# Kernel tuning notes

Hardware: AMD Instinct MI355X
Metric: run time of the kernel (lower is better)

Reference implementation:

```python
import jax, jax.numpy as jnp
import numpy as np

B, CH, IMG, P = 16, 3, 384, 16
D, HEADS, DH, MLP, DEPTH = 384, 6, 64, 1536, 6
INNER = HEADS * DH
PD = P * P * 5 * CH          # SPT patch dim = 3840
GRID = IMG // P              # 24
NP = GRID * GRID             # 576 patches
SEQ = NP + 1                 # +cls = 577


def layer_norm(x, g, b, eps=1e-5):
    mu = jnp.mean(x, axis=-1, keepdims=True)
    var = jnp.var(x, axis=-1, keepdims=True)
    return (x - mu) * jax.lax.rsqrt(var + eps) * g + b


def spt_shifts(x):
    # F.pad semantics: (left,right,top,bottom) with negative = crop
    s1 = jnp.pad(x, ((0, 0), (0, 0), (0, 0), (1, 0)))[:, :, :, :-1]  # (1,-1,0,0)
    s2 = jnp.pad(x, ((0, 0), (0, 0), (0, 0), (0, 1)))[:, :, :, 1:]   # (-1,1,0,0)
    s3 = jnp.pad(x, ((0, 0), (0, 0), (1, 0), (0, 0)))[:, :, :-1, :]  # (0,0,1,-1)
    s4 = jnp.pad(x, ((0, 0), (0, 0), (0, 1), (0, 0)))[:, :, 1:, :]   # (0,0,-1,1)
    return jnp.concatenate([x, s1, s2, s3, s4], axis=1)  # [b, 5c, H, W]


def patchify(x):
    # 'b c (h p1) (w p2) -> b (h w) (p1 p2 c)'
    b, c, _, _ = x.shape
    x = x.reshape(b, c, GRID, P, GRID, P)
    x = x.transpose(0, 2, 4, 3, 5, 1)  # b h w p1 p2 c
    return x.reshape(b, GRID * GRID, P * P * c)


def setup_inputs():
    key = jax.random.key(0)
    ks = jax.random.split(key, 16)
    img = jax.random.normal(ks[0], (B, CH, IMG, IMG), jnp.float32)
    spt_g = jnp.ones((PD,), jnp.float32)
    spt_b = jnp.zeros((PD,), jnp.float32)
    spt_w = jax.random.normal(ks[1], (PD, D), jnp.float32) * (1.0 / np.sqrt(PD))
    spt_bias = jnp.zeros((D,), jnp.float32)
    pos = jax.random.normal(ks[2], (1, SEQ, D), jnp.float32) * 0.02
    cls = jax.random.normal(ks[3], (1, 1, D), jnp.float32) * 0.02
    attn_g = jnp.ones((DEPTH, D), jnp.float32)
    attn_b = jnp.zeros((DEPTH, D), jnp.float32)
    temp = jnp.full((DEPTH,), np.log(DH ** -0.5), jnp.float32)
    wqkv = jax.random.normal(ks[4], (DEPTH, D, 3 * INNER), jnp.float32) * 0.02
    wout = jax.random.normal(ks[5], (DEPTH, INNER, D), jnp.float32) * 0.02
    bout = jnp.zeros((DEPTH, D), jnp.float32)
    ff_g = jnp.ones((DEPTH, D), jnp.float32)
    ff_b = jnp.zeros((DEPTH, D), jnp.float32)
    w1 = jax.random.normal(ks[6], (DEPTH, D, MLP), jnp.float32) * 0.02
    b1 = jnp.zeros((DEPTH, MLP), jnp.float32)
    w2 = jax.random.normal(ks[7], (DEPTH, MLP, D), jnp.float32) * 0.02
    b2 = jnp.zeros((DEPTH, D), jnp.float32)
    return {"img": img, "spt_g": spt_g, "spt_b": spt_b, "spt_w": spt_w,
            "spt_bias": spt_bias, "pos": pos, "cls": cls, "attn_g": attn_g,
            "attn_b": attn_b, "temp": temp, "wqkv": wqkv, "wout": wout,
            "bout": bout, "ff_g": ff_g, "ff_b": ff_b, "w1": w1, "b1": b1,
            "w2": w2, "b2": b2}


def vit_forward(img, spt_g, spt_b, spt_w, spt_bias, pos, cls, attn_g, attn_b,
                temp, wqkv, wout, bout, ff_g, ff_b, w1, b1, w2, b2):
    # SPT patch embedding
    x = patchify(spt_shifts(img))                      # [b, NP, PD]
    x = layer_norm(x, spt_g, spt_b) @ spt_w + spt_bias  # [b, NP, D]
    b = x.shape[0]
    cls_tok = jnp.broadcast_to(cls, (b, 1, D))
    x = jnp.concatenate([cls_tok, x], axis=1) + pos[:, :SEQ]

    eye = jnp.eye(SEQ, dtype=bool)
    neg = -jnp.finfo(x.dtype).max

    def block(x, p):
        ag, ab, t, wq, wo, bo, fg, fb, W1, B1, W2, B2 = p
        h = layer_norm(x, ag, ab)
        qkv = h @ wq                                   # [b, n, 3*inner]
        q, k, v = jnp.split(qkv, 3, axis=-1)
        q = q.reshape(b, SEQ, HEADS, DH).transpose(0, 2, 1, 3)
        k = k.reshape(b, SEQ, HEADS, DH).transpose(0, 2, 1, 3)
        v = v.reshape(b, SEQ, HEADS, DH).transpose(0, 2, 1, 3)
        dots = jnp.einsum('bhid,bhjd->bhij', q, k) * jnp.exp(t)
        dots = jnp.where(eye, neg, dots)               # diagonal mask (LSA)
        attn = jax.nn.softmax(dots, axis=-1)
        out = jnp.einsum('bhij,bhjd->bhid', attn, v)
        out = out.transpose(0, 2, 1, 3).reshape(b, SEQ, INNER)
        x = out @ wo + bo + x
        h = layer_norm(x, fg, fb)
        x = jax.nn.gelu(h @ W1 + B1, approximate=False) @ W2 + B2 + x
        return x, None

    params = (attn_g, attn_b, temp, wqkv, wout, bout, ff_g, ff_b, w1, b1, w2, b2)
    x, _ = jax.lax.scan(block, x, params)
    return x


def reference(img, spt_g, spt_b, spt_w, spt_bias, pos, cls, attn_g, attn_b,
              temp, wqkv, wout, bout, ff_g, ff_b, w1, b1, w2, b2):
    return vit_forward(img, spt_g, spt_b, spt_w, spt_bias, pos, cls, attn_g,
                       attn_b, temp, wqkv, wout, bout, ff_g, ff_b, w1, b1,
                       w2, b2)
```

## Files before the change

kernel.cpp:

```cpp
#include <hip/hip_runtime.h>

typedef unsigned short ushort_t;
typedef __bf16 bf16x8 __attribute__((ext_vector_type(8)));
typedef float f32x4 __attribute__((ext_vector_type(4)));

#define SEQ_ 577
#define D_ 384
#define NTOK (16 * 577)

enum { M_QKV = 0, M_OUT, M_MLP1, M_MLP2 };

__device__ inline float b2f(ushort_t u) {
    unsigned int x = ((unsigned int)u) << 16;
    float f; __builtin_memcpy(&f, &x, 4); return f;
}
__device__ inline ushort_t f2b(float f) {
    unsigned int x; __builtin_memcpy(&x, &f, 4);
    x = x + 0x7fffu + ((x >> 16) & 1u);
    return (ushort_t)(x >> 16);
}

__device__ void transpose_tile(const float* __restrict__ src,
                               ushort_t* __restrict__ dst,
                               int ldn, int ldk, int k0, int n0)
{
    __shared__ float t[64][65];
    const int tid = threadIdx.x;
    const int c = tid & 63, rr = tid >> 6;
#pragma unroll
    for (int i = 0; i < 16; i++) {
        int kl = rr + i * 4;
        t[kl][c] = src[(size_t)(k0 + kl) * ldn + n0 + c];
    }
    __syncthreads();
#pragma unroll
    for (int i = 0; i < 16; i++) {
        int nl = rr + i * 4;
        dst[(size_t)(n0 + nl) * ldk + k0 + c] = f2b(t[c][nl]);
    }
}

__global__ __launch_bounds__(256) void prep_spt_kernel(
    const float* __restrict__ w, ushort_t* __restrict__ wt)
{
    transpose_tile(w, wt, 384, 3840, blockIdx.x * 64, blockIdx.y * 64);
}

__global__ __launch_bounds__(256) void prep_all_kernel(
    const float* __restrict__ wqkv, const float* __restrict__ wout,
    const float* __restrict__ w1, const float* __restrict__ w2,
    ushort_t* __restrict__ W6)
{
    int id = blockIdx.x;
    int l = id / 432;
    int r = id - l * 432;
    ushort_t* qkv_t  = W6 + (size_t)l * 1769472;
    ushort_t* wout_t = qkv_t + 442368;
    ushort_t* w1_t   = wout_t + 147456;
    ushort_t* w2_t   = w1_t + 589824;
    const float* wq = wqkv + (size_t)l * 442368;
    const float* wo = wout + (size_t)l * 147456;
    const float* W1 = w1 + (size_t)l * 589824;
    const float* W2 = w2 + (size_t)l * 589824;
    if (r < 108) {
        int kt = r / 18, nt = r % 18;
        transpose_tile(wq, qkv_t, 1152, 384, kt * 64, nt * 64);
    } else if (r < 144) {
        r -= 108; int kt = r / 6, nt = r % 6;
        transpose_tile(wo, wout_t, 384, 384, kt * 64, nt * 64);
    } else if (r < 288) {
        r -= 144; int kt = r / 24, nt = r % 24;
        transpose_tile(W1, w1_t, 1536, 384, kt * 64, nt * 64);
    } else {
        r -= 288; int kt = r / 6, nt = r % 6;
        transpose_tile(W2, w2_t, 384, 1536, kt * 64, nt * 64);
    }
}

template <int MODE>
__global__ __launch_bounds__(256) void gemm128(
    const ushort_t* __restrict__ A, const ushort_t* __restrict__ Bt,
    ushort_t* __restrict__ Co, float* __restrict__ resid,
    const float* __restrict__ bias,
    int M, int K, int ldc)
{
    __shared__ __align__(16) ushort_t As[128][40];
    __shared__ __align__(16) ushort_t Bs[128][40];

    const int tid = threadIdx.x;
    const int rowBase = blockIdx.y * 128;
    const int colBase = blockIdx.x * 128;
    const int nk = K >> 5;

    const int lr = tid >> 2, lk = (tid & 3) * 8;
    const int wv = tid >> 6, lane = tid & 63;
    const int wm = (wv >> 1) * 64, wn = (wv & 1) * 64;
    const int m16 = lane & 15, q4 = lane >> 4, kb = q4 * 8;

    const ushort_t* pa0 = A + (size_t)(rowBase + lr) * K + lk;
    const ushort_t* pa1 = pa0 + (size_t)64 * K;
    const ushort_t* pb0 = Bt + (size_t)(colBase + lr) * K + lk;
    const ushort_t* pb1 = pb0 + (size_t)64 * K;

    f32x4 acc[4][4];
#pragma unroll
    for (int i = 0; i < 4; i++)
#pragma unroll
        for (int j = 0; j < 4; j++) acc[i][j] = (f32x4){0.f, 0.f, 0.f, 0.f};

    uint4 xa0 = *(const uint4*)pa0,        xa1 = *(const uint4*)pa1;
    uint4 xb0 = *(const uint4*)pb0,        xb1 = *(const uint4*)pb1;
    uint4 ya0 = *(const uint4*)(pa0 + 32), ya1 = *(const uint4*)(pa1 + 32);
    uint4 yb0 = *(const uint4*)(pb0 + 32), yb1 = *(const uint4*)(pb1 + 32);

    auto stage = [&](uint4& ra0, uint4& ra1, uint4& rb0, uint4& rb1, int ktNext) {
        __syncthreads();
        *(uint4*)&As[lr][lk] = ra0;
        *(uint4*)&As[64 + lr][lk] = ra1;
        *(uint4*)&Bs[lr][lk] = rb0;
        *(uint4*)&Bs[64 + lr][lk] = rb1;
        __syncthreads();
        if (ktNext < nk) {
            int off = ktNext * 32;
            ra0 = *(const uint4*)(pa0 + off);
            ra1 = *(const uint4*)(pa1 + off);
            rb0 = *(const uint4*)(pb0 + off);
            rb1 = *(const uint4*)(pb1 + off);
        }
        bf16x8 af[4], bf[4];
#pragma unroll
        for (int mt = 0; mt < 4; mt++) af[mt] = *(const bf16x8*)&As[wm + mt * 16 + m16][kb];
#pragma unroll
        for (int nt = 0; nt < 4; nt++) bf[nt] = *(const bf16x8*)&Bs[wn + nt * 16 + m16][kb];
#pragma unroll
        for (int mt = 0; mt < 4; mt++)
#pragma unroll
            for (int nt = 0; nt < 4; nt++)
                acc[mt][nt] = __builtin_amdgcn_mfma_f32_16x16x32_bf16(af[mt], bf[nt], acc[mt][nt], 0, 0, 0);
    };

    for (int kt = 0; kt < nk; kt += 2) {
        stage(xa0, xa1, xb0, xb1, kt + 2);
        stage(ya0, ya1, yb0, yb1, kt + 3);
    }

#pragma unroll
    for (int mt = 0; mt < 4; mt++)
#pragma unroll
        for (int nt = 0; nt < 4; nt++) {
            int col = colBase + wn + nt * 16 + m16;
#pragma unroll
            for (int r = 0; r < 4; r++) {
                int row = rowBase + wm + mt * 16 + q4 * 4 + r;
                if (row >= M) continue;
                float v = acc[mt][nt][r];
                if (MODE == M_QKV) {
                    Co[(size_t)row * ldc + col] = f2b(v);
                } else if (MODE == M_MLP1) {
                    float t = v + bias[col];
                    float gl = 0.5f * t * (1.0f + erff(t * 0.70710678118f));
                    Co[(size_t)row * ldc + col] = f2b(gl);
                } else if (MODE == M_OUT || MODE == M_MLP2) {
                    size_t o = (size_t)row * ldc + col;
                    resid[o] = resid[o] + v + bias[col];
                }
            }
        }
}

__global__ __launch_bounds__(256) void gemm64_spt(
    const ushort_t* __restrict__ A, const ushort_t* __restrict__ Bt,
    float* __restrict__ resid, const float* __restrict__ bias,
    const float* __restrict__ pos, int M, int K, int rowOff)
{
    __shared__ __align__(16) ushort_t As[64][40];
    __shared__ __align__(16) ushort_t Bs[64][40];

    const int tid = threadIdx.x;
    const int rowBase = blockIdx.y * 64;
    const int colBase = blockIdx.x * 64;
    const int nk = K >> 5;
    const int lr = tid >> 2, lk = (tid & 3) * 8;
    const int wv = tid >> 6, lane = tid & 63;
    const int wm = (wv >> 1) * 32, wn = (wv & 1) * 32;
    const int m16 = lane & 15, q4 = lane >> 4, kb = q4 * 8;

    const ushort_t* pa = A + (size_t)(rowBase + lr) * K + lk;
    const ushort_t* pb = Bt + (size_t)(colBase + lr) * K + lk;

    f32x4 acc[2][2];
#pragma unroll
    for (int i = 0; i < 2; i++)
#pragma unroll
        for (int j = 0; j < 2; j++) acc[i][j] = (f32x4){0.f, 0.f, 0.f, 0.f};

    uint4 xa = *(const uint4*)pa,        xb = *(const uint4*)pb;
    uint4 ya = *(const uint4*)(pa + 32), yb = *(const uint4*)(pb + 32);

    auto stage = [&](uint4& ra, uint4& rb, int ktNext) {
        __syncthreads();
        *(uint4*)&As[lr][lk] = ra;
        *(uint4*)&Bs[lr][lk] = rb;
        __syncthreads();
        if (ktNext < nk) {
            int off = ktNext * 32;
            ra = *(const uint4*)(pa + off);
            rb = *(const uint4*)(pb + off);
        }
        bf16x8 a0 = *(const bf16x8*)&As[wm + m16][kb];
        bf16x8 a1 = *(const bf16x8*)&As[wm + 16 + m16][kb];
        bf16x8 b0 = *(const bf16x8*)&Bs[wn + m16][kb];
        bf16x8 b1 = *(const bf16x8*)&Bs[wn + 16 + m16][kb];
        acc[0][0] = __builtin_amdgcn_mfma_f32_16x16x32_bf16(a0, b0, acc[0][0], 0, 0, 0);
        acc[0][1] = __builtin_amdgcn_mfma_f32_16x16x32_bf16(a0, b1, acc[0][1], 0, 0, 0);
        acc[1][0] = __builtin_amdgcn_mfma_f32_16x16x32_bf16(a1, b0, acc[1][0], 0, 0, 0);
        acc[1][1] = __builtin_amdgcn_mfma_f32_16x16x32_bf16(a1, b1, acc[1][1], 0, 0, 0);
    };

    for (int kt = 0; kt < nk; kt += 2) {
        stage(xa, xb, kt + 2);
        stage(ya, yb, kt + 3);
    }

#pragma unroll
    for (int im = 0; im < 2; im++)
#pragma unroll
        for (int in = 0; in < 2; in++) {
            int col = colBase + wn + in * 16 + m16;
#pragma unroll
            for (int r = 0; r < 4; r++) {
                int row = rowBase + wm + im * 16 + q4 * 4 + r;
                if (row >= M) continue;
                int grow = rowOff + row;
                int bb = grow / 576, p = grow - bb * 576;
                size_t o = ((size_t)(bb * SEQ_ + 1 + p)) * D_ + col;
                resid[o] = acc[im][in][r] + bias[col] + pos[(size_t)(1 + p) * D_ + col];
            }
        }
}

__global__ __launch_bounds__(256) void attn_kernel(
    const ushort_t* __restrict__ qkv, ushort_t* __restrict__ attn,
    const float* __restrict__ temp, int layer)
{
    const int qt = blockIdx.x;
    const int bh = blockIdx.y;
    const int b = bh / 6, hd = bh - b * 6;
    const int tid = threadIdx.x;
    const int wv = tid >> 6, lane = tid & 63;
    const int m16 = lane & 15, q4 = lane >> 4;
    const float sc2 = expf(temp[layer]) * 1.44269504f;

    __shared__ __align__(16) ushort_t Ks[64][72];
    __shared__ __align__(16) ushort_t Vt[64][72];
    __shared__ __align__(16) ushort_t Pw[4][16][72];

    const int qrow = qt * 64 + wv * 16 + m16;
    const int qtok = qrow < SEQ_ ? qrow : SEQ_ - 1;
    const ushort_t* qb = qkv + ((size_t)(b * SEQ_ + qtok)) * 1152 + hd * 64;
    bf16x8 qf0 = *(const bf16x8*)(qb + q4 * 8);
    bf16x8 qf1 = *(const bf16x8*)(qb + 32 + q4 * 8);

    f32x4 accO[4];
#pragma unroll
    for (int dt = 0; dt < 4; dt++) accO[dt] = (f32x4){0.f, 0.f, 0.f, 0.f};
    float l_r[4] = {0.f, 0.f, 0.f, 0.f};

    const int skey = tid >> 2;
    const int scol = (tid & 3) * 16;
    const int vp   = tid & 31;
    const int vdh  = (tid >> 5) * 8;

    for (int kt = 0; kt < 10; kt++) {
        int key = kt * 64 + skey;
        int gkey = key < SEQ_ ? key : 0;
        const ushort_t* kb_ = qkv + ((size_t)(b * SEQ_ + gkey)) * 1152 + 384 + hd * 64;
        uint4 kv0 = *(const uint4*)(kb_ + scol);
        uint4 kv1 = *(const uint4*)(kb_ + scol + 8);
        if (key >= SEQ_) { kv0 = (uint4){0, 0, 0, 0}; kv1 = kv0; }
        int vk0 = kt * 64 + 2 * vp;
        int t0 = vk0 < SEQ_ ? vk0 : 0;
        int t1 = vk0 + 1 < SEQ_ ? vk0 + 1 : 0;
        uint4 va = *(const uint4*)(qkv + ((size_t)(b * SEQ_ + t0)) * 1152 + 768 + hd * 64 + vdh);
        uint4 vb2 = *(const uint4*)(qkv + ((size_t)(b * SEQ_ + t1)) * 1152 + 768 + hd * 64 + vdh);
        if (vk0 >= SEQ_) va = (uint4){0, 0, 0, 0};
        if (vk0 + 1 >= SEQ_) vb2 = (uint4){0, 0, 0, 0};
        __syncthreads();
        *(uint4*)&Ks[skey][scol] = kv0;
        *(uint4*)&Ks[skey][scol + 8] = kv1;
        {
            const ushort_t* e0 = (const ushort_t*)&va;
            const ushort_t* e1 = (const ushort_t*)&vb2;
#pragma unroll
            for (int j = 0; j < 8; j++) {
                unsigned int pack = (unsigned int)e0[j] | ((unsigned int)e1[j] << 16);
                *(unsigned int*)&Vt[vdh + j][2 * vp] = pack;
            }
        }
        __syncthreads();

        f32x4 s[4];
#pragma unroll
        for (int ct = 0; ct < 4; ct++) {
            bf16x8 b0 = *(const bf16x8*)&Ks[ct * 16 + m16][q4 * 8];
            bf16x8 b1 = *(const bf16x8*)&Ks[ct * 16 + m16][32 + q4 * 8];
            f32x4 z = (f32x4){0.f, 0.f, 0.f, 0.f};
            z = __builtin_amdgcn_mfma_f32_16x16x32_bf16(qf0, b0, z, 0, 0, 0);
            z = __builtin_amdgcn_mfma_f32_16x16x32_bf16(qf1, b1, z, 0, 0, 0);
            s[ct] = z;
        }
        const int rowb = qt * 64 + wv * 16 + q4 * 4;
#pragma unroll
        for (int r = 0; r < 4; r++) {
            float rs = 0.f;
#pragma unroll
            for (int ct = 0; ct < 4; ct++) {
                int col = kt * 64 + ct * 16 + m16;
                float v = s[ct][r] * sc2;
                if (col >= SEQ_ || col == rowb + r) v = -1.0e30f;
                float p = __builtin_amdgcn_exp2f(v);
                s[ct][r] = p;
                rs += p;
            }
            rs += __shfl_xor(rs, 1);
            rs += __shfl_xor(rs, 2);
            rs += __shfl_xor(rs, 4);
            rs += __shfl_xor(rs, 8);
            l_r[r] += rs;
        }
#pragma unroll
        for (int ct = 0; ct < 4; ct++)
#pragma unroll
            for (int r = 0; r < 4; r++)
                Pw[wv][q4 * 4 + r][ct * 16 + m16] = f2b(s[ct][r]);
        bf16x8 pf0 = *(const bf16x8*)&Pw[wv][m16][q4 * 8];
        bf16x8 pf1 = *(const bf16x8*)&Pw[wv][m16][32 + q4 * 8];
#pragma unroll
        for (int dt = 0; dt < 4; dt++) {
            bf16x8 vb0 = *(const bf16x8*)&Vt[dt * 16 + m16][q4 * 8];
            bf16x8 vb1 = *(const bf16x8*)&Vt[dt * 16 + m16][32 + q4 * 8];
            f32x4 o = accO[dt];
            o = __builtin_amdgcn_mfma_f32_16x16x32_bf16(pf0, vb0, o, 0, 0, 0);
            o = __builtin_amdgcn_mfma_f32_16x16x32_bf16(pf1, vb1, o, 0, 0, 0);
            accO[dt] = o;
        }
    }

    const int rowb = qt * 64 + wv * 16 + q4 * 4;
#pragma unroll
    for (int r = 0; r < 4; r++) {
        int grow = rowb + r;
        if (grow >= SEQ_) continue;
        float inv = 1.f / l_r[r];
        ushort_t* op = attn + ((size_t)(b * SEQ_ + grow)) * 384 + hd * 64;
#pragma unroll
        for (int dt = 0; dt < 4; dt++)
            op[dt * 16 + m16] = f2b(accO[dt][r] * inv);
    }
}

__global__ __launch_bounds__(256) void spt_ln_kernel(
    const float* __restrict__ img, const float* __restrict__ gg,
    const float* __restrict__ bb_, ushort_t* __restrict__ Xn, int r0)
{
    int bp = r0 + blockIdx.x;
    int b = bp / 576, p = bp - b * 576;
    int ph = p / 24, pw = p - ph * 24;

    __shared__ float vals[3840];
    __shared__ float red[10];

    const int tid = threadIdx.x;
    const int p1 = tid >> 4, p2 = tid & 15;

    float s = 0.f, sq = 0.f;
#pragma unroll
    for (int plane = 0; plane < 15; plane++) {
        int g5 = plane / 3, ch = plane - g5 * 3;
        int row = ph * 16 + p1, col = pw * 16 + p2;
        if (g5 == 1) col -= 1;
        else if (g5 == 2) col += 1;
        else if (g5 == 3) row -= 1;
        else if (g5 == 4) row += 1;
        float v = 0.f;
        if (row >= 0 && row < 384 && col >= 0 && col < 384)
            v = img[((size_t)(b * 3 + ch) * 384 + row) * 384 + col];
        vals[tid * 15 + plane] = v;
        s += v; sq += v * v;
    }
#pragma unroll
    for (int off = 32; off > 0; off >>= 1) {
        s += __shfl_xor(s, off);
        sq += __shfl_xor(sq, off);
    }
    int wid = tid >> 6;
    if ((tid & 63) == 0) { red[wid] = s; red[4 + wid] = sq; }
    __syncthreads();
    if (tid == 0) {
        float S = red[0] + red[1] + red[2] + red[3];
        float Q = red[4] + red[5] + red[6] + red[7];
        float mean = S / 3840.f;
        float var = Q / 3840.f - mean * mean;
        red[8] = mean;
        red[9] = rsqrtf(var + 1e-5f);
    }
    __syncthreads();
    float mean = red[8], rstd = red[9];
#pragma unroll
    for (int i = 0; i < 15; i++) {
        int k = tid + i * 256;
        float v = (vals[k] - mean) * rstd * gg[k] + bb_[k];
        Xn[(size_t)blockIdx.x * 3840 + k] = f2b(v);
    }
}

__global__ __launch_bounds__(256) void ln_kernel(
    const float* __restrict__ x, const float* __restrict__ g,
    const float* __restrict__ b, ushort_t* __restrict__ h)
{
    int row = blockIdx.x * 4 + (threadIdx.x >> 6);
    int lane = threadIdx.x & 63;
    const float4* xr = (const float4*)(x + (size_t)row * 384);
    float4 a = xr[lane];
    float4 c = (lane < 32) ? xr[64 + lane] : make_float4(0.f, 0.f, 0.f, 0.f);
    float s = a.x + a.y + a.z + a.w + c.x + c.y + c.z + c.w;
    float sq = a.x * a.x + a.y * a.y + a.z * a.z + a.w * a.w
             + c.x * c.x + c.y * c.y + c.z * c.z + c.w * c.w;
#pragma unroll
    for (int off = 32; off > 0; off >>= 1) {
        s += __shfl_xor(s, off);
        sq += __shfl_xor(sq, off);
    }
    float mean = s / 384.f;
    float var = sq / 384.f - mean * mean;
    float rstd = rsqrtf(var + 1e-5f);
    const float4* g4 = (const float4*)g;
    const float4* b4 = (const float4*)b;
    ushort_t* hr = h + (size_t)row * 384;
    {
        float4 gv = g4[lane], bv = b4[lane];
        unsigned int lo = (unsigned int)f2b((a.x - mean) * rstd * gv.x + bv.x)
                        | ((unsigned int)f2b((a.y - mean) * rstd * gv.y + bv.y) << 16);
        unsigned int hi = (unsigned int)f2b((a.z - mean) * rstd * gv.z + bv.z)
                        | ((unsigned int)f2b((a.w - mean) * rstd * gv.w + bv.w) << 16);
        *(uint2*)&hr[lane * 4] = make_uint2(lo, hi);
    }
    if (lane < 32) {
        float4 gv = g4[64 + lane], bv = b4[64 + lane];
        unsigned int lo = (unsigned int)f2b((c.x - mean) * rstd * gv.x + bv.x)
                        | ((unsigned int)f2b((c.y - mean) * rstd * gv.y + bv.y) << 16);
        unsigned int hi = (unsigned int)f2b((c.z - mean) * rstd * gv.z + bv.z)
                        | ((unsigned int)f2b((c.w - mean) * rstd * gv.w + bv.w) << 16);
        *(uint2*)&hr[256 + lane * 4] = make_uint2(lo, hi);
    }
}

__global__ void cls_kernel(const float* __restrict__ cls,
                           const float* __restrict__ pos, float* __restrict__ x)
{
    int b = blockIdx.x, d = threadIdx.x;
    x[(size_t)b * SEQ_ * D_ + d] = cls[d] + pos[d];
}

extern "C" void kernel_launch(void* const* d_in, const int* in_sizes, int n_in,
                              void* d_out, int out_size, void* d_ws, size_t ws_size,
                              hipStream_t stream)
{
    const float* img      = (const float*)d_in[0];
    const float* spt_g    = (const float*)d_in[1];
    const float* spt_b    = (const float*)d_in[2];
    const float* spt_w    = (const float*)d_in[3];
    const float* spt_bias = (const float*)d_in[4];
    const float* pos      = (const float*)d_in[5];
    const float* clsp     = (const float*)d_in[6];
    const float* attn_g   = (const float*)d_in[7];
    const float* attn_b   = (const float*)d_in[8];
    const float* temp     = (const float*)d_in[9];
    const float* wqkv     = (const float*)d_in[10];
    const float* wout     = (const float*)d_in[11];
    const float* bout     = (const float*)d_in[12];
    const float* ff_g     = (const float*)d_in[13];
    const float* ff_b     = (const float*)d_in[14];
    const float* w1       = (const float*)d_in[15];
    const float* b1       = (const float*)d_in[16];
    const float* w2       = (const float*)d_in[17];
    const float* b2       = (const float*)d_in[18];

    float* x = (float*)d_out;

    char* base = (char*)d_ws;
    ushort_t* qkv   = (ushort_t*)base;
    ushort_t* attn  = (ushort_t*)(base + (size_t)NTOK * 1152 * 2);
    ushort_t* Xn    = (ushort_t*)base;
    ushort_t* gbuf  = (ushort_t*)base;
    ushort_t* spt_wt = (ushort_t*)(base + 23592960);
    char* p2 = base + (size_t)NTOK * 1536 * 2;
    ushort_t* h  = (ushort_t*)p2;
    char* p3 = p2 + (size_t)NTOK * 384 * 2;
    ushort_t* W6 = (ushort_t*)p3;

    prep_all_kernel<<<2592, 256, 0, stream>>>(wqkv, wout, w1, w2, W6);
    prep_spt_kernel<<<dim3(60, 6), 256, 0, stream>>>(spt_w, spt_wt);

    for (int c = 0; c < 3; c++) {
        int r0 = c * 3072;
        spt_ln_kernel<<<3072, 256, 0, stream>>>(img, spt_g, spt_b, Xn, r0);
        gemm64_spt<<<dim3(6, 48), 256, 0, stream>>>(
            Xn, spt_wt, x, spt_bias, pos, 3072, 3840, r0);
    }
    cls_kernel<<<16, 384, 0, stream>>>(clsp, pos, x);

    for (int l = 0; l < 6; l++) {
        ushort_t* qkv_t  = W6 + (size_t)l * 1769472;
        ushort_t* wout_t = qkv_t + 442368;
        ushort_t* w1_t   = wout_t + 147456;
        ushort_t* w2_t   = w1_t + 589824;
        ln_kernel<<<NTOK / 4, 256, 0, stream>>>(x, attn_g + l * 384, attn_b + l * 384, h);
        gemm128<M_QKV><<<dim3(9, 73), 256, 0, stream>>>(
            h, qkv_t, qkv, nullptr, nullptr, NTOK, 384, 1152);
        attn_kernel<<<dim3(10, 96), 256, 0, stream>>>(qkv, attn, temp, l);
        gemm128<M_OUT><<<dim3(3, 73), 256, 0, stream>>>(
            attn, wout_t, nullptr, x, bout + l * 384, NTOK, 384, 384);
        ln_kernel<<<NTOK / 4, 256, 0, stream>>>(x, ff_g + l * 384, ff_b + l * 384, h);
        gemm128<M_MLP1><<<dim3(12, 73), 256, 0, stream>>>(
            h, w1_t, gbuf, nullptr, b1 + l * 1536, NTOK, 384, 1536);
        gemm128<M_MLP2><<<dim3(3, 73), 256, 0, stream>>>(
            gbuf, w2_t, nullptr, x, b2 + l * 384, NTOK, 1536, 384);
    }
}
```

Before: 1.366 ms.

## Double-buffer LDS tiles in GEMM kernels to halve barriers per k-step

Both GEMM kernels move from a single LDS tile with two barriers per k-step to ping-pong LDS buffers. Each step writes the next tile into the other buffer while computing on the current one, with one barrier per step. The aim is to cut synchronisation stalls and overlap LDS writes and global loads with MFMA work. It doubles LDS use per block, which may lower occupancy, and the prologue and tail indexing become more intricate.

```diff
diff --git a/kernel.cpp b/kernel.cpp
--- a/kernel.cpp
+++ b/kernel.cpp
@@ -84,8 +84,8 @@
     const float* __restrict__ bias,
     int M, int K, int ldc)
 {
-    __shared__ __align__(16) ushort_t As[128][40];
-    __shared__ __align__(16) ushort_t Bs[128][40];
+    __shared__ __align__(16) ushort_t As[2][128][40];
+    __shared__ __align__(16) ushort_t Bs[2][128][40];
 
     const int tid = threadIdx.x;
     const int rowBase = blockIdx.y * 128;
@@ -108,30 +108,39 @@
 #pragma unroll
         for (int j = 0; j < 4; j++) acc[i][j] = (f32x4){0.f, 0.f, 0.f, 0.f};
 
-    uint4 xa0 = *(const uint4*)pa0,        xa1 = *(const uint4*)pa1;
-    uint4 xb0 = *(const uint4*)pb0,        xb1 = *(const uint4*)pb1;
-    uint4 ya0 = *(const uint4*)(pa0 + 32), ya1 = *(const uint4*)(pa1 + 32);
-    uint4 yb0 = *(const uint4*)(pb0 + 32), yb1 = *(const uint4*)(pb1 + 32);
-
-    auto stage = [&](uint4& ra0, uint4& ra1, uint4& rb0, uint4& rb1, int ktNext) {
-        __syncthreads();
-        *(uint4*)&As[lr][lk] = ra0;
-        *(uint4*)&As[64 + lr][lk] = ra1;
-        *(uint4*)&Bs[lr][lk] = rb0;
-        *(uint4*)&Bs[64 + lr][lk] = rb1;
-        __syncthreads();
-        if (ktNext < nk) {
-            int off = ktNext * 32;
-            ra0 = *(const uint4*)(pa0 + off);
-            ra1 = *(const uint4*)(pa1 + off);
-            rb0 = *(const uint4*)(pb0 + off);
-            rb1 = *(const uint4*)(pb1 + off);
-        }
+    uint4 U0, U1, U2, U3, V0, V1, V2, V3;
+    auto gloadU = [&](int kt) {
+        int off = kt * 32;
+        U0 = *(const uint4*)(pa0 + off);
+        U1 = *(const uint4*)(pa1 + off);
+        U2 = *(const uint4*)(pb0 + off);
+        U3 = *(const uint4*)(pb1 + off);
+    };
+    auto gloadV = [&](int kt) {
+        int off = kt * 32;
+        V0 = *(const uint4*)(pa0 + off);
+        V1 = *(const uint4*)(pa1 + off);
+        V2 = *(const uint4*)(pb0 + off);
+        V3 = *(const uint4*)(pb1 + off);
+    };
+    auto swriteU = [&](int buf) {
+        *(uint4*)&As[buf][lr][lk] = U0;
+        *(uint4*)&As[buf][64 + lr][lk] = U1;
+        *(uint4*)&Bs[buf][lr][lk] = U2;
+        *(uint4*)&Bs[buf][64 + lr][lk] = U3;
+    };
+    auto swriteV = [&](int buf) {
+        *(uint4*)&As[buf][lr][lk] = V0;
+        *(uint4*)&As[buf][64 + lr][lk] = V1;
+        *(uint4*)&Bs[buf][lr][lk] = V2;
+        *(uint4*)&Bs[buf][64 + lr][lk] = V3;
+    };
+    auto compute = [&](int buf) {
         bf16x8 af[4], bf[4];
 #pragma unroll
-        for (int mt = 0; mt < 4; mt++) af[mt] = *(const bf16x8*)&As[wm + mt * 16 + m16][kb];
-#pragma unroll
-        for (int nt = 0; nt < 4; nt++) bf[nt] = *(const bf16x8*)&Bs[wn + nt * 16 + m16][kb];
+        for (int mt = 0; mt < 4; mt++) af[mt] = *(const bf16x8*)&As[buf][wm + mt * 16 + m16][kb];
+#pragma unroll
+        for (int nt = 0; nt < 4; nt++) bf[nt] = *(const bf16x8*)&Bs[buf][wn + nt * 16 + m16][kb];
 #pragma unroll
         for (int mt = 0; mt < 4; mt++)
 #pragma unroll
@@ -139,9 +148,23 @@
                 acc[mt][nt] = __builtin_amdgcn_mfma_f32_16x16x32_bf16(af[mt], bf[nt], acc[mt][nt], 0, 0, 0);
     };
 
+    gloadU(0);
+    swriteU(0);
+    gloadU(1);
+    gloadV(2);
+    __syncthreads();
+
     for (int kt = 0; kt < nk; kt += 2) {
-        stage(xa0, xa1, xb0, xb1, kt + 2);
-        stage(ya0, ya1, yb0, yb1, kt + 3);
+        swriteU(1);
+        if (kt + 3 < nk) gloadU(kt + 3);
+        compute(0);
+        __syncthreads();
+        if (kt + 2 < nk) {
+            swriteV(0);
+            if (kt + 4 < nk) gloadV(kt + 4);
+        }
+        compute(1);
+        __syncthreads();
     }
 
 #pragma unroll
@@ -173,8 +196,8 @@
     float* __restrict__ resid, const float* __restrict__ bias,
     const float* __restrict__ pos, int M, int K, int rowOff)
 {
-    __shared__ __align__(16) ushort_t As[64][40];
-    __shared__ __align__(16) ushort_t Bs[64][40];
+    __shared__ __align__(16) ushort_t As[2][64][40];
+    __shared__ __align__(16) ushort_t Bs[2][64][40];
 
     const int tid = threadIdx.x;
     const int rowBase = blockIdx.y * 64;
@@ -194,32 +217,51 @@
 #pragma unroll
         for (int j = 0; j < 2; j++) acc[i][j] = (f32x4){0.f, 0.f, 0.f, 0.f};
 
-    uint4 xa = *(const uint4*)pa,        xb = *(const uint4*)pb;
-    uint4 ya = *(const uint4*)(pa + 32), yb = *(const uint4*)(pb + 32);
-
-    auto stage = [&](uint4& ra, uint4& rb, int ktNext) {
-        __syncthreads();
-        *(uint4*)&As[lr][lk] = ra;
-        *(uint4*)&Bs[lr][lk] = rb;
-        __syncthreads();
-        if (ktNext < nk) {
-            int off = ktNext * 32;
-            ra = *(const uint4*)(pa + off);
-            rb = *(const uint4*)(pb + off);
-        }
-        bf16x8 a0 = *(const bf16x8*)&As[wm + m16][kb];
-        bf16x8 a1 = *(const bf16x8*)&As[wm + 16 + m16][kb];
-        bf16x8 b0 = *(const bf16x8*)&Bs[wn + m16][kb];
-        bf16x8 b1 = *(const bf16x8*)&Bs[wn + 16 + m16][kb];
+    uint4 Ua, Ub, Va, Vb;
+    auto gloadU = [&](int kt) {
+        Ua = *(const uint4*)(pa + kt * 32);
+        Ub = *(const uint4*)(pb + kt * 32);
+    };
+    auto gloadV = [&](int kt) {
+        Va = *(const uint4*)(pa + kt * 32);
+        Vb = *(const uint4*)(pb + kt * 32);
+    };
+    auto swriteU = [&](int buf) {
+        *(uint4*)&As[buf][lr][lk] = Ua;
+        *(uint4*)&Bs[buf][lr][lk] = Ub;
+    };
+    auto swriteV = [&](int buf) {
+        *(uint4*)&As[buf][lr][lk] = Va;
+        *(uint4*)&Bs[buf][lr][lk] = Vb;
+    };
+    auto compute = [&](int buf) {
+        bf16x8 a0 = *(const bf16x8*)&As[buf][wm + m16][kb];
+        bf16x8 a1 = *(const bf16x8*)&As[buf][wm + 16 + m16][kb];
+        bf16x8 b0 = *(const bf16x8*)&Bs[buf][wn + m16][kb];
+        bf16x8 b1 = *(const bf16x8*)&Bs[buf][wn + 16 + m16][kb];
         acc[0][0] = __builtin_amdgcn_mfma_f32_16x16x32_bf16(a0, b0, acc[0][0], 0, 0, 0);
         acc[0][1] = __builtin_amdgcn_mfma_f32_16x16x32_bf16(a0, b1, acc[0][1], 0, 0, 0);
         acc[1][0] = __builtin_amdgcn_mfma_f32_16x16x32_bf16(a1, b0, acc[1][0], 0, 0, 0);
         acc[1][1] = __builtin_amdgcn_mfma_f32_16x16x32_bf16(a1, b1, acc[1][1], 0, 0, 0);
     };
 
+    gloadU(0);
+    swriteU(0);
+    gloadU(1);
+    gloadV(2);
+    __syncthreads();
+
     for (int kt = 0; kt < nk; kt += 2) {
-        stage(xa, xb, kt + 2);
-        stage(ya, yb, kt + 3);
+        swriteU(1);
+        if (kt + 3 < nk) gloadU(kt + 3);
+        compute(0);
+        __syncthreads();
+        if (kt + 2 < nk) {
+            swriteV(0);
+            if (kt + 4 < nk) gloadV(kt + 4);
+        }
+        compute(1);
+        __syncthreads();
     }
 
 #pragma unroll
```

Result: slower. 1.395 ms (+2.1%).
